# Performance work log

Measured on AMD Instinct MI355X. Metric: run time of the kernel, lower is better.

## Reference

```python
import jax, jax.numpy as jnp
import numpy as np

HIDDEN = 2048
N_HEADS = 32
N_KV_HEADS = 8
HEAD_DIM = HIDDEN // N_HEADS  # 64
KV_DIM = N_KV_HEADS * HEAD_DIM  # 512


def setup_inputs() -> dict:
    key = jax.random.key(0)
    ks = jax.random.split(key, 9)
    s = 1.0 / np.sqrt(HIDDEN)
    x = jax.random.normal(ks[0], (2, 2048, HIDDEN), dtype=jnp.float32)
    wq = jax.random.uniform(ks[1], (HIDDEN, HIDDEN), jnp.float32, -s, s)
    bq = jax.random.uniform(ks[2], (HIDDEN,), jnp.float32, -s, s)
    wk = jax.random.uniform(ks[3], (KV_DIM, HIDDEN), jnp.float32, -s, s)
    bk = jax.random.uniform(ks[4], (KV_DIM,), jnp.float32, -s, s)
    wv = jax.random.uniform(ks[5], (KV_DIM, HIDDEN), jnp.float32, -s, s)
    bv = jax.random.uniform(ks[6], (KV_DIM,), jnp.float32, -s, s)
    wo = jax.random.uniform(ks[7], (HIDDEN, HIDDEN), jnp.float32, -s, s)
    bo = jax.random.uniform(ks[8], (HIDDEN,), jnp.float32, -s, s)
    return {"x": x, "wq": wq, "bq": bq, "wk": wk, "bk": bk,
            "wv": wv, "bv": bv, "wo": wo, "bo": bo}


def reference(x, wq, bq, wk, bk, wv, bv, wo, bo):
    B, S, _ = x.shape
    group = N_HEADS // N_KV_HEADS  # 4
    # projections (torch Linear: x @ W.T + b)
    q = (x @ wq.T + bq).reshape(B, S, N_HEADS, HEAD_DIM).transpose(0, 2, 1, 3)      # [B,H,S,D]
    k = (x @ wk.T + bk).reshape(B, S, N_KV_HEADS, HEAD_DIM).transpose(0, 2, 1, 3)   # [B,Hk,S,D]
    v = (x @ wv.T + bv).reshape(B, S, N_KV_HEADS, HEAD_DIM).transpose(0, 2, 1, 3)
    # repeat_interleave KV heads to match query heads
    k = jnp.repeat(k, group, axis=1)  # [B,H,S,D]
    v = jnp.repeat(v, group, axis=1)
    scale = 1.0 / np.sqrt(HEAD_DIM).astype(np.float32)
    attn = jnp.einsum('bhqd,bhkd->bhqk', q, k) * scale  # [B,H,S,S]
    score = jax.nn.softmax(attn, axis=-1)
    out = jnp.einsum('bhqk,bhkd->bhqd', score, v)       # [B,H,S,D]
    out = out.transpose(0, 2, 1, 3).reshape(B, S, HIDDEN)
    return out @ wo.T + bo
```

## Files before the change

kernel.cpp:

```cpp
#include <hip/hip_runtime.h>

typedef __attribute__((ext_vector_type(8))) short bf16x8;
typedef __attribute__((ext_vector_type(4))) float f32x4;
typedef __attribute__((ext_vector_type(16))) float f32x16;

__device__ __forceinline__ short f2b(float f) {
  union { unsigned u; float f; } c;
  c.f = f;
  unsigned r = (c.u + 0x7FFFu + ((c.u >> 16) & 1u)) >> 16;
  return (short)r;
}

__device__ __forceinline__ int cvt_pk_bf16(float lo, float hi) {
  int r;
  asm("v_cvt_pk_bf16_f32 %0, %1, %2" : "=v"(r) : "v"(lo), "v"(hi));
  return r;
}

__device__ __forceinline__ void plswap(int& a, int& b) {
  asm volatile("v_permlane32_swap_b32 %0, %1" : "+v"(a), "+v"(b));
}

__device__ __forceinline__ void async16(const void* g, void* l) {
  __builtin_amdgcn_global_load_lds(
      (const __attribute__((address_space(1))) unsigned*)g,
      (__attribute__((address_space(3))) unsigned*)l, 16, 0, 0);
}

__global__ __launch_bounds__(256)
void f32_to_bf16(const float* __restrict__ src, short* __restrict__ dst, int n) {
  int i = (blockIdx.x * blockDim.x + threadIdx.x) * 4;
  if (i < n) {
    float4 v = *(const float4*)(src + i);
    short4 o;
    o.x = f2b(v.x); o.y = f2b(v.y); o.z = f2b(v.z); o.w = f2b(v.w);
    *(short4*)(dst + i) = o;
  }
}

template <bool F32OUT>
__global__ __launch_bounds__(256)
void gemm_bt_bias(const short* __restrict__ A, const short* __restrict__ Bw,
                  const float* __restrict__ bias, void* __restrict__ Cv,
                  int M, int N, int K) {
  __shared__ short lsA[128 * 32];
  __shared__ short lsB[128 * 32];
  const int tid  = threadIdx.x;
  const int wave = tid >> 6, lane = tid & 63;
  const int quad = lane >> 4, lrow = lane & 15;
  const int m0 = blockIdx.y * 128, n0 = blockIdx.x * 128;
  const int wm = (wave >> 1) * 64, wn = (wave & 1) * 64;

  f32x4 zero = {0.f, 0.f, 0.f, 0.f};
  f32x4 acc[4][4];
#pragma unroll
  for (int i = 0; i < 4; i++)
#pragma unroll
    for (int j = 0; j < 4; j++) acc[i][j] = zero;

  const int r0 = tid >> 2, c0 = (tid & 3) * 8;
  const short* Ab  = A  + (size_t)(m0 + r0) * K + c0;
  const short* Ab2 = A  + (size_t)(m0 + r0 + 64) * K + c0;
  const short* Bb  = Bw + (size_t)(n0 + r0) * K + c0;
  const short* Bb2 = Bw + (size_t)(n0 + r0 + 64) * K + c0;

  for (int k0 = 0; k0 < K; k0 += 32) {
    async16(Ab  + k0, lsA + tid * 8);
    async16(Ab2 + k0, lsA + (tid + 256) * 8);
    async16(Bb  + k0, lsB + tid * 8);
    async16(Bb2 + k0, lsB + (tid + 256) * 8);
    __syncthreads();

    bf16x8 af[4], bfr[4];
#pragma unroll
    for (int i = 0; i < 4; i++)
      af[i] = *(const bf16x8*)(lsA + (wm + i * 16 + lrow) * 32 + quad * 8);
#pragma unroll
    for (int j = 0; j < 4; j++)
      bfr[j] = *(const bf16x8*)(lsB + (wn + j * 16 + lrow) * 32 + quad * 8);
#pragma unroll
    for (int i = 0; i < 4; i++)
#pragma unroll
      for (int j = 0; j < 4; j++)
        acc[i][j] = __builtin_amdgcn_mfma_f32_16x16x32_bf16(af[i], bfr[j], acc[i][j], 0, 0, 0);
    __syncthreads();
  }

#pragma unroll
  for (int j = 0; j < 4; j++) {
    const int col = n0 + wn + j * 16 + lrow;
    const float bv = bias[col];
#pragma unroll
    for (int i = 0; i < 4; i++) {
      const int rowb = m0 + wm + i * 16 + quad * 4;
#pragma unroll
      for (int r = 0; r < 4; r++) {
        const float val = acc[i][j][r] + bv;
        if (F32OUT)
          ((float*)Cv)[(size_t)(rowb + r) * N + col] = val;
        else
          ((short*)Cv)[(size_t)(rowb + r) * N + col] = f2b(val);
      }
    }
  }
}

__global__ __launch_bounds__(256)
void gemm_qkv(const short* __restrict__ A, const short* __restrict__ Bw,
              const float* __restrict__ bq, const float* __restrict__ bk,
              const float* __restrict__ bv,
              short* __restrict__ Qo, short* __restrict__ Ko, short* __restrict__ Vo) {
  const int K = 2048;
  __shared__ short lsA[128 * 32];
  __shared__ short lsB[128 * 32];
  const int tid  = threadIdx.x;
  const int wave = tid >> 6, lane = tid & 63;
  const int quad = lane >> 4, lrow = lane & 15;
  const int m0 = blockIdx.y * 128, n0 = blockIdx.x * 128;
  const int wm = (wave >> 1) * 64, wn = (wave & 1) * 64;

  f32x4 zero = {0.f, 0.f, 0.f, 0.f};
  f32x4 acc[4][4];
#pragma unroll
  for (int i = 0; i < 4; i++)
#pragma unroll
    for (int j = 0; j < 4; j++) acc[i][j] = zero;

  const int r0 = tid >> 2, c0 = (tid & 3) * 8;
  const short* Ab  = A  + (size_t)(m0 + r0) * K + c0;
  const short* Ab2 = A  + (size_t)(m0 + r0 + 64) * K + c0;
  const short* Bb  = Bw + (size_t)(n0 + r0) * K + c0;
  const short* Bb2 = Bw + (size_t)(n0 + r0 + 64) * K + c0;

  for (int k0 = 0; k0 < K; k0 += 32) {
    async16(Ab  + k0, lsA + tid * 8);
    async16(Ab2 + k0, lsA + (tid + 256) * 8);
    async16(Bb  + k0, lsB + tid * 8);
    async16(Bb2 + k0, lsB + (tid + 256) * 8);
    __syncthreads();

    bf16x8 af[4], bfr[4];
#pragma unroll
    for (int i = 0; i < 4; i++)
      af[i] = *(const bf16x8*)(lsA + (wm + i * 16 + lrow) * 32 + quad * 8);
#pragma unroll
    for (int j = 0; j < 4; j++)
      bfr[j] = *(const bf16x8*)(lsB + (wn + j * 16 + lrow) * 32 + quad * 8);
#pragma unroll
    for (int i = 0; i < 4; i++)
#pragma unroll
      for (int j = 0; j < 4; j++)
        acc[i][j] = __builtin_amdgcn_mfma_f32_16x16x32_bf16(af[i], bfr[j], acc[i][j], 0, 0, 0);
    __syncthreads();
  }

  short* base; int stride, coff; const float* bias;
  if (n0 < 2048)      { base = Qo; stride = 2048; bias = bq; coff = 0; }
  else if (n0 < 2560) { base = Ko; stride = 512;  bias = bk; coff = 2048; }
  else                { base = Vo; stride = 512;  bias = bv; coff = 2560; }
  const float qs = (n0 < 2048) ? 0.18033688011112043f : 1.0f;

#pragma unroll
  for (int j = 0; j < 4; j++) {
    const int lc = n0 + wn + j * 16 + lrow - coff;
    const float bvv = bias[lc];
#pragma unroll
    for (int i = 0; i < 4; i++) {
      const int rowb = m0 + wm + i * 16 + quad * 4;
#pragma unroll
      for (int r = 0; r < 4; r++)
        base[(size_t)(rowb + r) * stride + lc] = f2b((acc[i][j][r] + bvv) * qs);
    }
  }
}

#define S_LEN 2048
#define HID   2048
#define KVD   512
#define ST    72

__global__ __launch_bounds__(256)
void gqa_flash(const short* __restrict__ Q, const short* __restrict__ Kb,
               const short* __restrict__ Vb, short* __restrict__ O) {
  __shared__ __align__(16) short lsK[64 * ST];
  __shared__ __align__(16) short lsVt[64 * ST];
  __shared__ float lsum[4][32];

  const int tid  = threadIdx.x;
  const int wave = tid >> 6, lane = tid & 63;
  const int l31  = lane & 31, hl = lane >> 5;

  const int d  = blockIdx.x + (blockIdx.y << 6);
  const int by = ((d & 7) << 1) | (d >> 9);
  const int qb = (d >> 3) & 63;
  const int b = by >> 3, kvh = by & 7;
  const int h = kvh * 4 + wave;
  const int q0 = qb * 32;

  const short* Qrow = Q + (size_t)(b * S_LEN + q0 + l31) * HID + h * 64 + hl * 8;
  bf16x8 qf[4];
#pragma unroll
  for (int f = 0; f < 4; f++) qf[f] = *(const bf16x8*)(Qrow + f * 16);

  f32x16 o0, o1;
#pragma unroll
  for (int i = 0; i < 16; i++) { o0[i] = 0.f; o1[i] = 0.f; }
  float lloc = 0.f;

  const short* Kp = Kb + (size_t)b * S_LEN * KVD + kvh * 64;
  const short* Vp = Vb + (size_t)b * S_LEN * KVD + kvh * 64;

  const int keyA = tid >> 3, chK = (tid & 7) * 8;
  const int kpV = tid & 31, dcV = (tid >> 5) * 8;

  bf16x8 kf0 = *(const bf16x8*)(Kp + (size_t)keyA * KVD + chK);
  bf16x8 kf1 = *(const bf16x8*)(Kp + (size_t)(keyA + 32) * KVD + chK);
  bf16x8 vf0 = *(const bf16x8*)(Vp + (size_t)(2 * kpV) * KVD + dcV);
  bf16x8 vf1 = *(const bf16x8*)(Vp + (size_t)(2 * kpV + 1) * KVD + dcV);

  for (int k0 = 0; k0 < S_LEN; k0 += 64) {
    *(bf16x8*)(lsK + keyA * ST + chK) = kf0;
    *(bf16x8*)(lsK + (keyA + 32) * ST + chK) = kf1;
#pragma unroll
    for (int jj = 0; jj < 8; jj++) {
      unsigned pk = (unsigned)(unsigned short)vf0[jj] |
                    ((unsigned)(unsigned short)vf1[jj] << 16);
      *(unsigned*)(lsVt + (dcV + jj) * ST + 2 * kpV) = pk;
    }
    __syncthreads();

    const int kn = (k0 + 64) & (S_LEN - 1);
    kf0 = *(const bf16x8*)(Kp + (size_t)(kn + keyA) * KVD + chK);
    kf1 = *(const bf16x8*)(Kp + (size_t)(kn + keyA + 32) * KVD + chK);
    vf0 = *(const bf16x8*)(Vp + (size_t)(kn + 2 * kpV) * KVD + dcV);
    vf1 = *(const bf16x8*)(Vp + (size_t)(kn + 2 * kpV + 1) * KVD + dcV);

    f32x16 s0, s1;
#pragma unroll
    for (int i = 0; i < 16; i++) { s0[i] = 0.f; s1[i] = 0.f; }
    __builtin_amdgcn_s_setprio(1);
#pragma unroll
    for (int f = 0; f < 4; f++) {
      bf16x8 ka = *(const bf16x8*)(lsK + l31 * ST + f * 16 + hl * 8);
      bf16x8 kb = *(const bf16x8*)(lsK + (32 + l31) * ST + f * 16 + hl * 8);
      s0 = __builtin_amdgcn_mfma_f32_32x32x16_bf16(ka, qf[f], s0, 0, 0, 0);
      s1 = __builtin_amdgcn_mfma_f32_32x32x16_bf16(kb, qf[f], s1, 0, 0, 0);
    }
    __builtin_amdgcn_s_setprio(0);

#pragma unroll
    for (int i = 0; i < 16; i++) {
      s0[i] = __builtin_amdgcn_exp2f(s0[i]);
      s1[i] = __builtin_amdgcn_exp2f(s1[i]);
    }
    {
      f32x16 ps = s0 + s1;
      float a0 = (ps[0] + ps[1]) + (ps[2] + ps[3]);
      float a1 = (ps[4] + ps[5]) + (ps[6] + ps[7]);
      float a2 = (ps[8] + ps[9]) + (ps[10] + ps[11]);
      float a3 = (ps[12] + ps[13]) + (ps[14] + ps[15]);
      lloc += (a0 + a1) + (a2 + a3);
    }
    int P2[2][8];
#pragma unroll
    for (int qq = 0; qq < 8; qq++) {
      P2[0][qq] = cvt_pk_bf16(s0[2 * qq], s0[2 * qq + 1]);
      P2[1][qq] = cvt_pk_bf16(s1[2 * qq], s1[2 * qq + 1]);
    }

    __builtin_amdgcn_s_setprio(1);
#pragma unroll
    for (int t = 0; t < 4; t++) {
      const int j = t >> 1, b0 = (t & 1) * 4;
      int w0 = P2[j][b0 + 0], w2 = P2[j][b0 + 2];
      int w1 = P2[j][b0 + 1], w3 = P2[j][b0 + 3];
      plswap(w0, w2);
      plswap(w1, w3);
      union { unsigned u[4]; bf16x8 v; } pa;
      pa.u[0] = (unsigned)w0; pa.u[1] = (unsigned)w1;
      pa.u[2] = (unsigned)w2; pa.u[3] = (unsigned)w3;
      bf16x8 bv0 = *(const bf16x8*)(lsVt + l31 * ST + t * 16 + hl * 8);
      bf16x8 bv1 = *(const bf16x8*)(lsVt + (32 + l31) * ST + t * 16 + hl * 8);
      o0 = __builtin_amdgcn_mfma_f32_32x32x16_bf16(pa.v, bv0, o0, 0, 0, 0);
      o1 = __builtin_amdgcn_mfma_f32_32x32x16_bf16(pa.v, bv1, o1, 0, 0, 0);
    }
    __builtin_amdgcn_s_setprio(0);
    __syncthreads();
  }

  const float lfull = lloc + __shfl(lloc, lane ^ 32);
  if (lane < 32) lsum[wave][lane] = lfull;
#pragma unroll
  for (int r = 0; r < 16; r++) {
    const int qrow = (r & 3) + 8 * (r >> 2) + 4 * hl;
    const float rl = 1.0f / lsum[wave][qrow];
    short* op = O + (size_t)(b * S_LEN + q0 + qrow) * HID + h * 64 + l31;
    op[0]  = f2b(o0[r] * rl);
    op[32] = f2b(o1[r] * rl);
  }
}

extern "C" void kernel_launch(void* const* d_in, const int* in_sizes, int n_in,
                              void* d_out, int out_size, void* d_ws, size_t ws_size,
                              hipStream_t stream) {
  const float* x  = (const float*)d_in[0];
  const float* wq = (const float*)d_in[1];
  const float* bq = (const float*)d_in[2];
  const float* wk = (const float*)d_in[3];
  const float* bk = (const float*)d_in[4];
  const float* wv = (const float*)d_in[5];
  const float* bv = (const float*)d_in[6];
  const float* wo = (const float*)d_in[7];
  const float* bo = (const float*)d_in[8];
  float* out = (float*)d_out;

  short* xb  = (short*)d_ws;
  short* wqb = xb  + (size_t)4096 * 2048;
  short* wkb = wqb + (size_t)2048 * 2048;
  short* wvb = wkb + (size_t)512 * 2048;
  short* wob = wvb + (size_t)512 * 2048;
  short* Qb  = wob + (size_t)2048 * 2048;
  short* Kb  = Qb  + (size_t)4096 * 2048;
  short* Vb  = Kb  + (size_t)4096 * 512;
  short* AO  = Vb  + (size_t)4096 * 512;

  dim3 blk(256);
  f32_to_bf16<<<4096 * 2048 / 1024, blk, 0, stream>>>(x,  xb,  4096 * 2048);
  f32_to_bf16<<<2048 * 2048 / 1024, blk, 0, stream>>>(wq, wqb, 2048 * 2048);
  f32_to_bf16<<< 512 * 2048 / 1024, blk, 0, stream>>>(wk, wkb, 512 * 2048);
  f32_to_bf16<<< 512 * 2048 / 1024, blk, 0, stream>>>(wv, wvb, 512 * 2048);
  f32_to_bf16<<<2048 * 2048 / 1024, blk, 0, stream>>>(wo, wob, 2048 * 2048);

  gemm_qkv<<<dim3(3072 / 128, 4096 / 128), blk, 0, stream>>>(xb, wqb, bq, bk, bv, Qb, Kb, Vb);
  gqa_flash<<<dim3(2048 / 32, 16), blk, 0, stream>>>(Qb, Kb, Vb, AO);
  gemm_bt_bias<true><<<dim3(2048 / 128, 4096 / 128), blk, 0, stream>>>(AO, wob, bo, out, 4096, 2048, 2048);
}
```

Before: 334.6 us.

## Merge f32-to-bf16 conversions into one launch and tighten attention inner loop

Replaces five separate f32-to-bf16 conversion launches with one kernel that picks the source tensor by index range. This relies on the bf16 workspace buffers being laid out contiguously. The attention loop now builds transposed V pairs with v_perm_b32 instead of shift/or packing, and computes the row-sum reduction with packed v_pk_add_f32. Together these cut launch overhead and VALU instruction count in the flash-attention inner loop.

```diff
diff --git a/kernel.cpp b/kernel.cpp
--- a/kernel.cpp
+++ b/kernel.cpp
@@ -3,6 +3,7 @@
 typedef __attribute__((ext_vector_type(8))) short bf16x8;
 typedef __attribute__((ext_vector_type(4))) float f32x4;
 typedef __attribute__((ext_vector_type(16))) float f32x16;
+typedef __attribute__((ext_vector_type(2))) float f32x2;
 
 __device__ __forceinline__ short f2b(float f) {
   union { unsigned u; float f; } c;
@@ -21,6 +22,18 @@
   asm volatile("v_permlane32_swap_b32 %0, %1" : "+v"(a), "+v"(b));
 }
 
+__device__ __forceinline__ f32x2 pk_add(f32x2 a, f32x2 b) {
+  f32x2 d;
+  asm("v_pk_add_f32 %0, %1, %2" : "=v"(d) : "v"(a), "v"(b));
+  return d;
+}
+
+__device__ __forceinline__ unsigned permb(unsigned s0, unsigned s1, unsigned sel) {
+  unsigned d;
+  asm("v_perm_b32 %0, %1, %2, %3" : "=v"(d) : "v"(s0), "v"(s1), "s"(sel));
+  return d;
+}
+
 __device__ __forceinline__ void async16(const void* g, void* l) {
   __builtin_amdgcn_global_load_lds(
       (const __attribute__((address_space(1))) unsigned*)g,
@@ -28,14 +41,21 @@
 }
 
 __global__ __launch_bounds__(256)
-void f32_to_bf16(const float* __restrict__ src, short* __restrict__ dst, int n) {
-  int i = (blockIdx.x * blockDim.x + threadIdx.x) * 4;
-  if (i < n) {
-    float4 v = *(const float4*)(src + i);
-    short4 o;
-    o.x = f2b(v.x); o.y = f2b(v.y); o.z = f2b(v.z); o.w = f2b(v.w);
-    *(short4*)(dst + i) = o;
-  }
+void conv_all(const float* __restrict__ x,  const float* __restrict__ wq,
+              const float* __restrict__ wk, const float* __restrict__ wv,
+              const float* __restrict__ wo, short* __restrict__ dst) {
+  const size_t M = 1048576;
+  size_t i = ((size_t)blockIdx.x * 256 + threadIdx.x) * 4;
+  const float* src; size_t off;
+  if (i < 8 * M)       { src = x;  off = 0; }
+  else if (i < 12 * M) { src = wq; off = 8 * M; }
+  else if (i < 13 * M) { src = wk; off = 12 * M; }
+  else if (i < 14 * M) { src = wv; off = 13 * M; }
+  else                 { src = wo; off = 14 * M; }
+  float4 v = *(const float4*)(src + (i - off));
+  short4 o;
+  o.x = f2b(v.x); o.y = f2b(v.y); o.z = f2b(v.z); o.w = f2b(v.w);
+  *(short4*)(dst + i) = o;
 }
 
 template <bool F32OUT>
@@ -221,11 +241,16 @@
   for (int k0 = 0; k0 < S_LEN; k0 += 64) {
     *(bf16x8*)(lsK + keyA * ST + chK) = kf0;
     *(bf16x8*)(lsK + (keyA + 32) * ST + chK) = kf1;
-#pragma unroll
-    for (int jj = 0; jj < 8; jj++) {
-      unsigned pk = (unsigned)(unsigned short)vf0[jj] |
-                    ((unsigned)(unsigned short)vf1[jj] << 16);
-      *(unsigned*)(lsVt + (dcV + jj) * ST + 2 * kpV) = pk;
+    {
+      const unsigned* u0 = (const unsigned*)&vf0;
+      const unsigned* u1 = (const unsigned*)&vf1;
+#pragma unroll
+      for (int jw = 0; jw < 4; jw++) {
+        unsigned lo = permb(u1[jw], u0[jw], 0x05040100u);
+        unsigned hi = permb(u1[jw], u0[jw], 0x07060302u);
+        *(unsigned*)(lsVt + (dcV + 2 * jw)     * ST + 2 * kpV) = lo;
+        *(unsigned*)(lsVt + (dcV + 2 * jw + 1) * ST + 2 * kpV) = hi;
+      }
     }
     __syncthreads();
 
@@ -254,12 +279,21 @@
       s1[i] = __builtin_amdgcn_exp2f(s1[i]);
     }
     {
-      f32x16 ps = s0 + s1;
-      float a0 = (ps[0] + ps[1]) + (ps[2] + ps[3]);
-      float a1 = (ps[4] + ps[5]) + (ps[6] + ps[7]);
-      float a2 = (ps[8] + ps[9]) + (ps[10] + ps[11]);
-      float a3 = (ps[12] + ps[13]) + (ps[14] + ps[15]);
-      lloc += (a0 + a1) + (a2 + a3);
+      const f32x2* p0 = (const f32x2*)&s0;
+      const f32x2* p1 = (const f32x2*)&s1;
+      f32x2 t0 = pk_add(p0[0], p1[0]);
+      f32x2 t1 = pk_add(p0[1], p1[1]);
+      f32x2 t2 = pk_add(p0[2], p1[2]);
+      f32x2 t3 = pk_add(p0[3], p1[3]);
+      f32x2 t4 = pk_add(p0[4], p1[4]);
+      f32x2 t5 = pk_add(p0[5], p1[5]);
+      f32x2 t6 = pk_add(p0[6], p1[6]);
+      f32x2 t7 = pk_add(p0[7], p1[7]);
+      t0 = pk_add(t0, t4); t1 = pk_add(t1, t5);
+      t2 = pk_add(t2, t6); t3 = pk_add(t3, t7);
+      t0 = pk_add(t0, t2); t1 = pk_add(t1, t3);
+      t0 = pk_add(t0, t1);
+      lloc += t0.x + t0.y;
     }
     int P2[2][8];
 #pragma unroll
@@ -325,11 +359,7 @@
   short* AO  = Vb  + (size_t)4096 * 512;
 
   dim3 blk(256);
-  f32_to_bf16<<<4096 * 2048 / 1024, blk, 0, stream>>>(x,  xb,  4096 * 2048);
-  f32_to_bf16<<<2048 * 2048 / 1024, blk, 0, stream>>>(wq, wqb, 2048 * 2048);
-  f32_to_bf16<<< 512 * 2048 / 1024, blk, 0, stream>>>(wk, wkb, 512 * 2048);
-  f32_to_bf16<<< 512 * 2048 / 1024, blk, 0, stream>>>(wv, wvb, 512 * 2048);
-  f32_to_bf16<<<2048 * 2048 / 1024, blk, 0, stream>>>(wo, wob, 2048 * 2048);
+  conv_all<<<18 * 1048576 / 1024, blk, 0, stream>>>(x, wq, wk, wv, wo, xb);
 
   gemm_qkv<<<dim3(3072 / 128, 4096 / 128), blk, 0, stream>>>(xb, wqb, bq, bk, bv, Qb, Kb, Vb);
   gqa_flash<<<dim3(2048 / 32, 16), blk, 0, stream>>>(Qb, Kb, Vb, AO);
```

Result: faster. 320.1 us (-4.3%).
